# Kernel optimization log

Measured on AMD Instinct MI355X. Metric: run time of the kernel, lower is better.

## Reference

```python
import jax, jax.numpy as jnp
import numpy as np

OUT = 7       # roi_pooling_output_size
SR = 2        # bilinear samples per bin side (torchvision default is adaptive; fixed here)
STRIDES = (4, 8, 16, 32)
LEVELS = (2, 3, 4, 5)  # log2(strides)


def _roi_align(feat, boxes, bidx, scale):
    """roi_align, aligned=False. feat [B,C,H,W], boxes [N,4] xyxy image coords."""
    N = boxes.shape[0]
    C, H, W = feat.shape[1], feat.shape[2], feat.shape[3]
    x1 = boxes[:, 0] * scale; y1 = boxes[:, 1] * scale
    x2 = boxes[:, 2] * scale; y2 = boxes[:, 3] * scale
    rw = jnp.maximum(x2 - x1, 1.0); rh = jnp.maximum(y2 - y1, 1.0)
    g = (jnp.arange(SR, dtype=feat.dtype) + 0.5) / SR
    off = (jnp.arange(OUT, dtype=feat.dtype)[:, None] + g[None, :]).reshape(-1)  # [OUT*SR]
    ys = y1[:, None] + off[None, :] * (rh / OUT)[:, None]  # [N, OUT*SR]
    xs = x1[:, None] + off[None, :] * (rw / OUT)[:, None]
    M = OUT * SR
    y = jnp.broadcast_to(ys[:, :, None], (N, M, M)).reshape(N, M * M)
    x = jnp.broadcast_to(xs[:, None, :], (N, M, M)).reshape(N, M * M)
    valid = (y > -1.0) & (y < H) & (x > -1.0) & (x < W)
    y = jnp.clip(y, 0.0, H - 1); x = jnp.clip(x, 0.0, W - 1)
    y0f = jnp.floor(y); x0f = jnp.floor(x)
    y0 = y0f.astype(jnp.int32); x0 = x0f.astype(jnp.int32)
    yb = jnp.minimum(y0 + 1, H - 1); xb = jnp.minimum(x0 + 1, W - 1)
    ly = y - y0f; lx = x - x0f

    def gat(yi, xi):
        return feat[bidx[:, None], :, yi, xi]  # [N, P, C]

    v = (((1 - ly) * (1 - lx))[..., None] * gat(y0, x0)
         + ((1 - ly) * lx)[..., None] * gat(y0, xb)
         + (ly * (1 - lx))[..., None] * gat(yb, x0)
         + (ly * lx)[..., None] * gat(yb, xb))
    v = jnp.where(valid[..., None], v, 0.0)
    v = v.reshape(N, OUT, SR, OUT, SR, C).mean(axis=(2, 4))  # avg samples per bin
    return v.transpose(0, 3, 1, 2)  # [N, C, OUT, OUT]


def _forward(feat2, feat3, feat4, feat5, rois, W_fc1, b_fc1, W_fc2, b_fc2,
             W_cls, b_cls, W_reg, b_reg):
    feats = (feat2, feat3, feat4, feat5)
    BS, R = rois.shape[0], rois.shape[1]
    N = BS * R
    boxes = rois.reshape(N, 4)
    bidx = jnp.repeat(jnp.arange(BS, dtype=jnp.int32), R)
    w = boxes[:, 2] - boxes[:, 0]
    h = boxes[:, 3] - boxes[:, 1]
    # FPN level routing: floor(4 + log2(sqrt(wh)/224 + 1e-6)); unclamped, as in source
    lv = jnp.floor(4.0 + jnp.log2(jnp.sqrt(w * h) / 224.0 + 1e-6))
    C = feat2.shape[1]
    roi_feats = jnp.zeros((N, C, OUT, OUT), dtype=feat2.dtype)
    for f, s, l in zip(feats, STRIDES, LEVELS):
        rf = _roi_align(f, boxes, bidx, 1.0 / s)
        roi_feats = roi_feats + jnp.where((lv == l)[:, None, None, None], rf, 0.0)
    x = roi_feats.reshape(N, -1)                    # [N, 12544]
    x = jax.nn.relu(x @ W_fc1.T + b_fc1)            # roi_head fc1
    x = jax.nn.relu(x @ W_fc2.T + b_fc2)            # roi_head fc2
    cls_pred = (x @ W_cls.T + b_cls).reshape(BS, R, -1)
    reg_pred = (x @ W_reg.T + b_reg).reshape(BS, R, -1, 4)
    return cls_pred, reg_pred


def setup_inputs() -> dict:
    key = jax.random.key(0)
    ks = jax.random.split(key, 12)
    BS, R, C = 2, 512, 256
    IMG = 800.0
    inp = {}
    for i, (name, s) in enumerate(zip(['feat2', 'feat3', 'feat4', 'feat5'],
                                      [200, 100, 50, 25])):
        inp[name] = jax.random.normal(ks[i], (BS, C, s, s), dtype=jnp.float32)
    # realistic ROIs: uniform centers, log-uniform sizes in [32, 512] px
    ctr = jax.random.uniform(ks[4], (BS, R, 2), minval=0.0, maxval=IMG)
    sz = jnp.exp(jax.random.uniform(ks[5], (BS, R, 2),
                                    minval=jnp.log(32.0), maxval=jnp.log(512.0)))
    x1y1 = jnp.clip(ctr - sz / 2, 0.0, IMG)
    x2y2 = jnp.clip(ctr + sz / 2, 0.0, IMG)
    inp['rois'] = jnp.concatenate([x1y1, x2y2], axis=-1)
    D, F, NCLS = 1024, C * OUT * OUT, 80
    inp['W_fc1'] = 0.01 * jax.random.normal(ks[6], (D, F), dtype=jnp.float32)
    inp['b_fc1'] = jnp.zeros((D,), dtype=jnp.float32)
    inp['W_fc2'] = 0.01 * jax.random.normal(ks[7], (D, D), dtype=jnp.float32)
    inp['b_fc2'] = jnp.zeros((D,), dtype=jnp.float32)
    inp['W_cls'] = 0.01 * jax.random.normal(ks[8], (NCLS + 1, D), dtype=jnp.float32)
    inp['b_cls'] = jnp.zeros((NCLS + 1,), dtype=jnp.float32)
    inp['W_reg'] = 0.01 * jax.random.normal(ks[9], (NCLS * 4, D), dtype=jnp.float32)
    inp['b_reg'] = jnp.zeros((NCLS * 4,), dtype=jnp.float32)
    return inp


def reference(feat2, feat3, feat4, feat5, rois, W_fc1, b_fc1, W_fc2, b_fc2,
              W_cls, b_cls, W_reg, b_reg):
    return _forward(feat2, feat3, feat4, feat5, rois, W_fc1, b_fc1, W_fc2, b_fc2,
                    W_cls, b_cls, W_reg, b_reg)
```

## Files before the change

kernel.cpp:

```cpp
#include <hip/hip_runtime.h>

typedef __bf16 bf16_t;
typedef __bf16 bf16x8 __attribute__((ext_vector_type(8)));
typedef __bf16 bf16x4v __attribute__((ext_vector_type(4)));
typedef float f32x4 __attribute__((ext_vector_type(4)));

#define GLDS16(g, l)                                                            \
  __builtin_amdgcn_global_load_lds((const __attribute__((address_space(1))) void*)(g), \
                                   (__attribute__((address_space(3))) void*)(l), 16, 0, 0)

__global__ __launch_bounds__(256) void cvt_bf16_kernel(const float* __restrict__ x,
                                                       bf16_t* __restrict__ y, int n4) {
  int i = blockIdx.x * 256 + threadIdx.x;
  if (i >= n4) return;
  float4 v = ((const float4*)x)[i];
  union { bf16_t b[4]; uint2 u; } p;
  p.b[0] = (bf16_t)v.x; p.b[1] = (bf16_t)v.y; p.b[2] = (bf16_t)v.z; p.b[3] = (bf16_t)v.w;
  ((uint2*)y)[i] = p.u;
}

__global__ __launch_bounds__(256) void build_cat_kernel(const float* __restrict__ Wc,
                                                        const float* __restrict__ bc,
                                                        const float* __restrict__ Wr,
                                                        const float* __restrict__ br,
                                                        bf16_t* __restrict__ Wcat,
                                                        float* __restrict__ bcat) {
  int i = blockIdx.x * 256 + threadIdx.x;
  int row = i >> 10, col = i & 1023;
  float v = 0.0f;
  if (row < 81) v = Wc[row * 1024 + col];
  else if (row < 401) v = Wr[(row - 81) * 1024 + col];
  Wcat[i] = (bf16_t)v;
  if (i < 448) bcat[i] = (i < 81) ? bc[i] : ((i < 401) ? br[i - 81] : 0.0f);
}

__global__ __launch_bounds__(256) void nchw_to_nhwc_bf16(const float* __restrict__ src,
                                                         bf16_t* __restrict__ dst, int P) {
  __shared__ float tile[64 * 65];
  const int t = threadIdx.x;
  const int p0 = blockIdx.x * 64, c0 = blockIdx.y * 64, b = blockIdx.z;
  const float* s = src + (size_t)(b * 256 + c0) * P;
#pragma unroll
  for (int it = 0; it < 16; ++it) {
    const int ch = it * 4 + (t >> 6);
    const int px = t & 63;
    float v = 0.0f;
    if (p0 + px < P) v = s[(size_t)ch * P + p0 + px];
    tile[ch * 65 + px] = v;
  }
  __syncthreads();
  bf16_t* d = dst + ((size_t)b * P + p0) * 256 + c0;
#pragma unroll
  for (int it = 0; it < 4; ++it) {
    const int px = it * 16 + (t >> 4);
    const int ch4 = (t & 15) * 4;
    if (p0 + px < P) {
      union { bf16_t bb[4]; uint2 u; } pk;
#pragma unroll
      for (int k2 = 0; k2 < 4; k2++) pk.bb[k2] = (bf16_t)tile[(ch4 + k2) * 65 + px];
      *(uint2*)&d[(size_t)px * 256 + ch4] = pk.u;
    }
  }
}

__global__ __launch_bounds__(256) void permute_w1(const float* __restrict__ W1,
                                                  bf16_t* __restrict__ W1p) {
  __shared__ bf16_t lds[49 * 258];
  const int t = threadIdx.x;
  const float* src = W1 + (size_t)blockIdx.x * 12544;
  for (int it = 0; it < 49; ++it) {
    const int j = it * 256 + t;
    const int c = j / 49;
    const int bin = j - c * 49;
    lds[bin * 258 + c] = (bf16_t)src[j];
  }
  __syncthreads();
  bf16_t* dst = W1p + (size_t)blockIdx.x * 12544;
  for (int j4 = t; j4 < 3136; j4 += 256) {
    const int bin = j4 >> 6;
    const int c = (j4 & 63) * 4;
    union { bf16_t bb[4]; uint2 u; } pk;
#pragma unroll
    for (int k2 = 0; k2 < 4; k2++) pk.bb[k2] = lds[bin * 258 + c + k2];
    ((uint2*)dst)[j4] = pk.u;
  }
}

__global__ __launch_bounds__(256) void roi_align_nhwc(const bf16_t* __restrict__ fb2,
                                                      const bf16_t* __restrict__ fb3,
                                                      const bf16_t* __restrict__ fb4,
                                                      const bf16_t* __restrict__ fb5,
                                                      const float* __restrict__ rois,
                                                      bf16_t* __restrict__ A) {
  const int n = blockIdx.x;
  const int t = threadIdx.x;
  const int b = n >> 9;
  const float4 box = ((const float4*)rois)[n];
  const float w = box.z - box.x, h = box.w - box.y;
  const int lv = (int)floorf(4.0f + log2f(sqrtf(w * h) / 224.0f + 1e-6f));
  bf16_t* Ar = A + (size_t)n * 12544;

  if (lv < 2 || lv > 5) {
    uint2 z; z.x = 0; z.y = 0;
    for (int j = t; j < 3136; j += 256) ((uint2*)Ar)[j] = z;
    return;
  }

  const bf16_t* F; int H, W; float scale;
  if (lv == 2)      { F = fb2; H = 200; W = 200; scale = 0.25f; }
  else if (lv == 3) { F = fb3; H = 100; W = 100; scale = 0.125f; }
  else if (lv == 4) { F = fb4; H = 50;  W = 50;  scale = 0.0625f; }
  else              { F = fb5; H = 25;  W = 25;  scale = 0.03125f; }
  F += (size_t)b * H * W * 256;

  __shared__ int   s_x0[14], s_xb[14], s_y0w[14], s_ybw[14];
  __shared__ float s_wx0[14], s_wx1[14], s_wy0[14], s_wy1[14];

  const float x1s = box.x * scale, y1s = box.y * scale;
  const float x2s = box.z * scale, y2s = box.w * scale;
  const float rw = fmaxf(x2s - x1s, 1.0f), rh = fmaxf(y2s - y1s, 1.0f);
  const float bwx = rw * (1.0f / 7.0f), bwy = rh * (1.0f / 7.0f);

  if (t < 14) {
    const int i2 = t >> 1, j = t & 1;
    const float off = (float)i2 + ((float)j + 0.5f) * 0.5f;
    float x = x1s + off * bwx;
    float vx = (x > -1.0f && x < (float)W) ? 1.0f : 0.0f;
    x = fminf(fmaxf(x, 0.0f), (float)(W - 1));
    float x0f = floorf(x);
    int x0 = (int)x0f;
    s_x0[t] = x0; s_xb[t] = min(x0 + 1, W - 1);
    float lx = x - x0f;
    s_wx0[t] = (1.0f - lx) * vx; s_wx1[t] = lx * vx;
    float y = y1s + off * bwy;
    float vy = (y > -1.0f && y < (float)H) ? 1.0f : 0.0f;
    y = fminf(fmaxf(y, 0.0f), (float)(H - 1));
    float y0f = floorf(y);
    int y0 = (int)y0f;
    s_y0w[t] = y0 * W; s_ybw[t] = min(y0 + 1, H - 1) * W;
    float ly = y - y0f;
    s_wy0[t] = (1.0f - ly) * vy; s_wy1[t] = ly * vy;
  }
  __syncthreads();

  const int wv = t >> 6, l = t & 63;
  const int c4 = l * 4;
  for (int bin = wv; bin < 49; bin += 4) {
    const int by = bin / 7, bx = bin - by * 7;
    float a0 = 0, a1 = 0, a2 = 0, a3 = 0;
#pragma unroll
    for (int sa = 0; sa < 2; sa++) {
      const int my = 2 * by + sa;
      const int y0w = s_y0w[my], ybw = s_ybw[my];
      const float wy0 = s_wy0[my], wy1 = s_wy1[my];
#pragma unroll
      for (int sb = 0; sb < 2; sb++) {
        const int mx = 2 * bx + sb;
        const int x0 = s_x0[mx], xb = s_xb[mx];
        const float w00 = wy0 * s_wx0[mx], w01 = wy0 * s_wx1[mx];
        const float w10 = wy1 * s_wx0[mx], w11 = wy1 * s_wx1[mx];
        bf16x4v v00 = *(const bf16x4v*)&F[(size_t)(y0w + x0) * 256 + c4];
        bf16x4v v01 = *(const bf16x4v*)&F[(size_t)(y0w + xb) * 256 + c4];
        bf16x4v v10 = *(const bf16x4v*)&F[(size_t)(ybw + x0) * 256 + c4];
        bf16x4v v11 = *(const bf16x4v*)&F[(size_t)(ybw + xb) * 256 + c4];
        a0 += w00 * (float)v00[0] + w01 * (float)v01[0] + w10 * (float)v10[0] + w11 * (float)v11[0];
        a1 += w00 * (float)v00[1] + w01 * (float)v01[1] + w10 * (float)v10[1] + w11 * (float)v11[1];
        a2 += w00 * (float)v00[2] + w01 * (float)v01[2] + w10 * (float)v10[2] + w11 * (float)v11[2];
        a3 += w00 * (float)v00[3] + w01 * (float)v01[3] + w10 * (float)v10[3] + w11 * (float)v11[3];
      }
    }
    union { bf16_t bb[4]; uint2 u; } pk;
    pk.bb[0] = (bf16_t)(a0 * 0.25f);
    pk.bb[1] = (bf16_t)(a1 * 0.25f);
    pk.bb[2] = (bf16_t)(a2 * 0.25f);
    pk.bb[3] = (bf16_t)(a3 * 0.25f);
    *(uint2*)&Ar[bin * 256 + c4] = pk.u;
  }
}

__global__ __launch_bounds__(256, 2) void gemm1_splitk(const bf16_t* __restrict__ A,
                                                       const bf16_t* __restrict__ B,
                                                       float* __restrict__ Cp) {
  __shared__ __align__(16) bf16_t As[128 * 32];
  __shared__ __align__(16) bf16_t Bs[128 * 32];
  const int t = threadIdx.x;
  const int w = t >> 6, l = t & 63;
  const int bm = blockIdx.x * 128, bn = blockIdx.y * 128;
  const int K = 12544;
  const int k0 = blockIdx.z * 1568;
  const int row1 = t >> 2, kc = (t & 3) * 8;
  const bf16_t* gA1 = A + (size_t)(bm + row1) * K + k0 + kc;
  const bf16_t* gA2 = gA1 + (size_t)64 * K;
  const bf16_t* gB1 = B + (size_t)(bn + row1) * K + k0 + kc;
  const bf16_t* gB2 = gB1 + (size_t)64 * K;
  bf16_t* lA1 = As + w * 512;
  bf16_t* lA2 = As + 2048 + w * 512;
  bf16_t* lB1 = Bs + w * 512;
  bf16_t* lB2 = Bs + 2048 + w * 512;
  const int wm = (w >> 1) * 64, wn = (w & 1) * 64;
  const int rA = l & 15, kq = (l >> 4) * 8;
  f32x4 acc[4][4] = {};

  for (int kk = 0; kk < 49; ++kk) {
    GLDS16(gA1, lA1); GLDS16(gA2, lA2);
    GLDS16(gB1, lB1); GLDS16(gB2, lB2);
    gA1 += 32; gA2 += 32; gB1 += 32; gB2 += 32;
    __syncthreads();
    bf16x8 a[4], b[4];
#pragma unroll
    for (int i = 0; i < 4; i++) {
      a[i] = *(const bf16x8*)&As[(wm + i * 16 + rA) * 32 + kq];
      b[i] = *(const bf16x8*)&Bs[(wn + i * 16 + rA) * 32 + kq];
    }
#pragma unroll
    for (int i = 0; i < 4; i++)
#pragma unroll
      for (int j = 0; j < 4; j++)
        acc[i][j] = __builtin_amdgcn_mfma_f32_16x16x32_bf16(a[i], b[j], acc[i][j], 0, 0, 0);
    __syncthreads();
  }

  const int q = l >> 4, cc = l & 15;
  float* Co = Cp + ((size_t)blockIdx.z << 20);
#pragma unroll
  for (int i = 0; i < 4; i++) {
#pragma unroll
    for (int j = 0; j < 4; j++) {
      const int col = bn + wn + j * 16 + cc;
      const int r0 = bm + wm + i * 16 + q * 4;
#pragma unroll
      for (int r = 0; r < 4; r++)
        Co[(size_t)(r0 + r) * 1024 + col] = acc[i][j][r];
    }
  }
}

__global__ __launch_bounds__(256) void reduce_fc1(const float* __restrict__ Cp,
                                                  const float* __restrict__ bias,
                                                  bf16_t* __restrict__ X) {
  const int i4 = blockIdx.x * 256 + threadIdx.x;
  const float4* C4 = (const float4*)Cp;
  float4 s = C4[i4];
#pragma unroll
  for (int z = 1; z < 8; z++) {
    float4 v = C4[(size_t)z * 262144 + i4];
    s.x += v.x; s.y += v.y; s.z += v.z; s.w += v.w;
  }
  const float4 bv = *(const float4*)&bias[(i4 & 255) * 4];
  union { bf16_t bb[4]; uint2 u; } pk;
  pk.bb[0] = (bf16_t)fmaxf(s.x + bv.x, 0.0f);
  pk.bb[1] = (bf16_t)fmaxf(s.y + bv.y, 0.0f);
  pk.bb[2] = (bf16_t)fmaxf(s.z + bv.z, 0.0f);
  pk.bb[3] = (bf16_t)fmaxf(s.w + bv.w, 0.0f);
  ((uint2*)X)[i4] = pk.u;
}

template <int MODE>
__global__ __launch_bounds__(256) void gemm_bt(const bf16_t* __restrict__ A,
                                               const bf16_t* __restrict__ B,
                                               const float* __restrict__ bias,
                                               void* __restrict__ out,
                                               int M, int N, int K) {
  __shared__ __align__(16) bf16_t As[64 * 32];
  __shared__ __align__(16) bf16_t Bs[64 * 32];
  const int t = threadIdx.x;
  const int wv = t >> 6, l = t & 63;
  const int bm = blockIdx.x * 64, bn = blockIdx.y * 64;
  const int wm = (wv >> 1) * 32, wn = (wv & 1) * 32;

  const int srow = t >> 2;
  const int skc = (t & 3) * 8;
  const bf16_t* ga = A + (size_t)(bm + srow) * K + skc;
  const bf16_t* gb = B + (size_t)(bn + srow) * K + skc;

  uint4 ra = *(const uint4*)ga;
  uint4 rb = *(const uint4*)gb;
  f32x4 acc[2][2] = {};

  const int nIter = K >> 5;
  const int rA = l & 15;
  const int kq = (l >> 4) << 3;
  for (int i = 0; i < nIter; ++i) {
    ga += 32; gb += 32;
    *(uint4*)&As[srow * 32 + skc] = ra;
    *(uint4*)&Bs[srow * 32 + skc] = rb;
    __syncthreads();
    if (i + 1 < nIter) { ra = *(const uint4*)ga; rb = *(const uint4*)gb; }
    bf16x8 a0 = *(const bf16x8*)&As[(wm + rA) * 32 + kq];
    bf16x8 a1 = *(const bf16x8*)&As[(wm + 16 + rA) * 32 + kq];
    bf16x8 b0 = *(const bf16x8*)&Bs[(wn + rA) * 32 + kq];
    bf16x8 b1 = *(const bf16x8*)&Bs[(wn + 16 + rA) * 32 + kq];
    acc[0][0] = __builtin_amdgcn_mfma_f32_16x16x32_bf16(a0, b0, acc[0][0], 0, 0, 0);
    acc[0][1] = __builtin_amdgcn_mfma_f32_16x16x32_bf16(a0, b1, acc[0][1], 0, 0, 0);
    acc[1][0] = __builtin_amdgcn_mfma_f32_16x16x32_bf16(a1, b0, acc[1][0], 0, 0, 0);
    acc[1][1] = __builtin_amdgcn_mfma_f32_16x16x32_bf16(a1, b1, acc[1][1], 0, 0, 0);
    __syncthreads();
  }

  const int q = l >> 4;
  const int cc = l & 15;
#pragma unroll
  for (int i2 = 0; i2 < 2; i2++) {
#pragma unroll
    for (int j2 = 0; j2 < 2; j2++) {
      const int col = bn + wn + j2 * 16 + cc;
      const int row0 = bm + wm + i2 * 16 + q * 4;
      const float bv = bias[col];
#pragma unroll
      for (int r = 0; r < 4; r++) {
        float v = acc[i2][j2][r] + bv;
        const int row = row0 + r;
        if (MODE == 0) {
          v = fmaxf(v, 0.0f);
          ((bf16_t*)out)[(size_t)row * N + col] = (bf16_t)v;
        } else {
          if (col < 81)       ((float*)out)[(size_t)row * 81 + col] = v;
          else if (col < 401) ((float*)out)[82944 + (size_t)row * 320 + (col - 81)] = v;
        }
      }
    }
  }
}

extern "C" void kernel_launch(void* const* d_in, const int* in_sizes, int n_in,
                              void* d_out, int out_size, void* d_ws, size_t ws_size,
                              hipStream_t stream) {
  const float* f2   = (const float*)d_in[0];
  const float* f3   = (const float*)d_in[1];
  const float* f4   = (const float*)d_in[2];
  const float* f5   = (const float*)d_in[3];
  const float* rois = (const float*)d_in[4];
  const float* W1   = (const float*)d_in[5];
  const float* b1   = (const float*)d_in[6];
  const float* W2   = (const float*)d_in[7];
  const float* b2   = (const float*)d_in[8];
  const float* Wc   = (const float*)d_in[9];
  const float* bc   = (const float*)d_in[10];
  const float* Wr   = (const float*)d_in[11];
  const float* br   = (const float*)d_in[12];

  char* ws = (char*)d_ws;
  bf16_t* Ab   = (bf16_t*)(ws);
  bf16_t* W1b  = (bf16_t*)(ws + 25690112);
  bf16_t* X1b  = (bf16_t*)(ws + 51380224);
  bf16_t* W2b  = (bf16_t*)(ws + 53477376);
  bf16_t* X2b  = (bf16_t*)(ws + 55574528);
  bf16_t* Wcb  = (bf16_t*)(ws + 57671680);
  float*  bcat = (float*)(ws + 58589184);
  bf16_t* FT   = (bf16_t*)(ws + 58591232);
  float*  Cp   = (float*)(ws + 58591232);
  bf16_t* FT2 = FT;
  bf16_t* FT3 = FT + 20480000;
  bf16_t* FT4 = FT + 25600000;
  bf16_t* FT5 = FT + 26880000;

  nchw_to_nhwc_bf16<<<dim3(625, 4, 2), 256, 0, stream>>>(f2, FT2, 40000);
  nchw_to_nhwc_bf16<<<dim3(157, 4, 2), 256, 0, stream>>>(f3, FT3, 10000);
  nchw_to_nhwc_bf16<<<dim3(40, 4, 2), 256, 0, stream>>>(f4, FT4, 2500);
  nchw_to_nhwc_bf16<<<dim3(10, 4, 2), 256, 0, stream>>>(f5, FT5, 625);
  cvt_bf16_kernel<<<1024, 256, 0, stream>>>(W2, W2b, 262144);
  build_cat_kernel<<<1792, 256, 0, stream>>>(Wc, bc, Wr, br, Wcb, bcat);
  permute_w1<<<1024, 256, 0, stream>>>(W1, W1b);
  roi_align_nhwc<<<1024, 256, 0, stream>>>(FT2, FT3, FT4, FT5, rois, Ab);

  gemm1_splitk<<<dim3(8, 8, 8), 256, 0, stream>>>(Ab, W1b, Cp);
  reduce_fc1<<<1024, 256, 0, stream>>>(Cp, b1, X1b);
  gemm_bt<0><<<dim3(16, 16), 256, 0, stream>>>(X1b, W2b, b2, (void*)X2b, 1024, 1024, 1024);
  gemm_bt<1><<<dim3(16, 7), 256, 0, stream>>>(X2b, Wcb, bcat, d_out, 1024, 448, 1024);
}
```

Baseline: 355.0 us.

## Merge prep kernels, fuse split-K reduction into GEMM1, swizzle LDS layouts

All preprocessing launches (feature transposes, W1 permute, W2 and classifier weight conversion, counter reset) are merged into one kernel that dispatches on block index. The separate split-K reduce kernel is removed. The last block to finish each output tile, found with an atomic counter, now sums the partials and applies bias and ReLU. An XOR swizzle of the LDS k-chunk offsets is added in both GEMMs to cut bank conflicts. These changes target launch overhead, an extra pass over the partial buffer and LDS conflicts, at the cost of threadfence/atomic ordering and a serialized tail for the last block per tile.

```diff
diff --git a/kernel.cpp b/kernel.cpp
--- a/kernel.cpp
+++ b/kernel.cpp
@@ -9,80 +9,98 @@
   __builtin_amdgcn_global_load_lds((const __attribute__((address_space(1))) void*)(g), \
                                    (__attribute__((address_space(3))) void*)(l), 16, 0, 0)
 
-__global__ __launch_bounds__(256) void cvt_bf16_kernel(const float* __restrict__ x,
-                                                       bf16_t* __restrict__ y, int n4) {
-  int i = blockIdx.x * 256 + threadIdx.x;
-  if (i >= n4) return;
-  float4 v = ((const float4*)x)[i];
-  union { bf16_t b[4]; uint2 u; } p;
-  p.b[0] = (bf16_t)v.x; p.b[1] = (bf16_t)v.y; p.b[2] = (bf16_t)v.z; p.b[3] = (bf16_t)v.w;
-  ((uint2*)y)[i] = p.u;
-}
-
-__global__ __launch_bounds__(256) void build_cat_kernel(const float* __restrict__ Wc,
-                                                        const float* __restrict__ bc,
-                                                        const float* __restrict__ Wr,
-                                                        const float* __restrict__ br,
-                                                        bf16_t* __restrict__ Wcat,
-                                                        float* __restrict__ bcat) {
-  int i = blockIdx.x * 256 + threadIdx.x;
-  int row = i >> 10, col = i & 1023;
-  float v = 0.0f;
-  if (row < 81) v = Wc[row * 1024 + col];
-  else if (row < 401) v = Wr[(row - 81) * 1024 + col];
-  Wcat[i] = (bf16_t)v;
-  if (i < 448) bcat[i] = (i < 81) ? bc[i] : ((i < 401) ? br[i - 81] : 0.0f);
-}
-
-__global__ __launch_bounds__(256) void nchw_to_nhwc_bf16(const float* __restrict__ src,
-                                                         bf16_t* __restrict__ dst, int P) {
-  __shared__ float tile[64 * 65];
+__global__ __launch_bounds__(256) void prep_all(const float* __restrict__ f2,
+                                                const float* __restrict__ f3,
+                                                const float* __restrict__ f4,
+                                                const float* __restrict__ f5,
+                                                const float* __restrict__ W1,
+                                                const float* __restrict__ W2,
+                                                const float* __restrict__ Wc,
+                                                const float* __restrict__ bc,
+                                                const float* __restrict__ Wr,
+                                                const float* __restrict__ br,
+                                                bf16_t* __restrict__ FT2,
+                                                bf16_t* __restrict__ FT3,
+                                                bf16_t* __restrict__ FT4,
+                                                bf16_t* __restrict__ FT5,
+                                                bf16_t* __restrict__ W1p,
+                                                bf16_t* __restrict__ W2b,
+                                                bf16_t* __restrict__ Wcb,
+                                                float* __restrict__ bcat,
+                                                int* __restrict__ cnt) {
+  __shared__ __align__(16) char smraw[25344];
+  const int bid = blockIdx.x;
   const int t = threadIdx.x;
-  const int p0 = blockIdx.x * 64, c0 = blockIdx.y * 64, b = blockIdx.z;
-  const float* s = src + (size_t)(b * 256 + c0) * P;
-#pragma unroll
-  for (int it = 0; it < 16; ++it) {
-    const int ch = it * 4 + (t >> 6);
-    const int px = t & 63;
+
+  if (bid < 6656) {
+    float* tile = (float*)smraw;
+    const float* src; bf16_t* dst; int P, rel, ptiles;
+    if (bid < 5000)      { src = f2; dst = FT2; P = 40000; rel = bid;        ptiles = 625; }
+    else if (bid < 6256) { src = f3; dst = FT3; P = 10000; rel = bid - 5000; ptiles = 157; }
+    else if (bid < 6576) { src = f4; dst = FT4; P = 2500;  rel = bid - 6256; ptiles = 40; }
+    else                 { src = f5; dst = FT5; P = 625;   rel = bid - 6576; ptiles = 10; }
+    const int pt = rel % ptiles;
+    const int cb = (rel / ptiles) & 3;
+    const int b = rel / (ptiles * 4);
+    const int p0 = pt * 64, c0 = cb * 64;
+    const float* s = src + (size_t)(b * 256 + c0) * P;
+#pragma unroll
+    for (int it = 0; it < 16; ++it) {
+      const int ch = it * 4 + (t >> 6);
+      const int px = t & 63;
+      float v = 0.0f;
+      if (p0 + px < P) v = s[(size_t)ch * P + p0 + px];
+      tile[ch * 65 + px] = v;
+    }
+    __syncthreads();
+    bf16_t* d = dst + ((size_t)b * P + p0) * 256 + c0;
+#pragma unroll
+    for (int it = 0; it < 4; ++it) {
+      const int px = it * 16 + (t >> 4);
+      const int ch4 = (t & 15) * 4;
+      if (p0 + px < P) {
+        union { bf16_t bb[4]; uint2 u; } pk;
+#pragma unroll
+        for (int k2 = 0; k2 < 4; k2++) pk.bb[k2] = (bf16_t)tile[(ch4 + k2) * 65 + px];
+        *(uint2*)&d[(size_t)px * 256 + ch4] = pk.u;
+      }
+    }
+  } else if (bid < 7680) {
+    bf16_t* pw = (bf16_t*)smraw;
+    const int row = bid - 6656;
+    const float* src = W1 + (size_t)row * 12544;
+    for (int it = 0; it < 49; ++it) {
+      const int j = it * 256 + t;
+      const int c = j / 49;
+      const int bin = j - c * 49;
+      pw[bin * 258 + c] = (bf16_t)src[j];
+    }
+    __syncthreads();
+    bf16_t* dst = W1p + (size_t)row * 12544;
+    for (int j4 = t; j4 < 3136; j4 += 256) {
+      const int bin = j4 >> 6;
+      const int c = (j4 & 63) * 4;
+      union { bf16_t bb[4]; uint2 u; } pk;
+#pragma unroll
+      for (int k2 = 0; k2 < 4; k2++) pk.bb[k2] = pw[bin * 258 + c + k2];
+      ((uint2*)dst)[j4] = pk.u;
+    }
+  } else if (bid < 8704) {
+    const int i = (bid - 7680) * 256 + t;
+    float4 v = ((const float4*)W2)[i];
+    union { bf16_t b[4]; uint2 u; } p;
+    p.b[0] = (bf16_t)v.x; p.b[1] = (bf16_t)v.y; p.b[2] = (bf16_t)v.z; p.b[3] = (bf16_t)v.w;
+    ((uint2*)W2b)[i] = p.u;
+  } else if (bid < 10496) {
+    const int i = (bid - 8704) * 256 + t;
+    const int row = i >> 10, col = i & 1023;
     float v = 0.0f;
-    if (p0 + px < P) v = s[(size_t)ch * P + p0 + px];
-    tile[ch * 65 + px] = v;
-  }
-  __syncthreads();
-  bf16_t* d = dst + ((size_t)b * P + p0) * 256 + c0;
-#pragma unroll
-  for (int it = 0; it < 4; ++it) {
-    const int px = it * 16 + (t >> 4);
-    const int ch4 = (t & 15) * 4;
-    if (p0 + px < P) {
-      union { bf16_t bb[4]; uint2 u; } pk;
-#pragma unroll
-      for (int k2 = 0; k2 < 4; k2++) pk.bb[k2] = (bf16_t)tile[(ch4 + k2) * 65 + px];
-      *(uint2*)&d[(size_t)px * 256 + ch4] = pk.u;
-    }
-  }
-}
-
-__global__ __launch_bounds__(256) void permute_w1(const float* __restrict__ W1,
-                                                  bf16_t* __restrict__ W1p) {
-  __shared__ bf16_t lds[49 * 258];
-  const int t = threadIdx.x;
-  const float* src = W1 + (size_t)blockIdx.x * 12544;
-  for (int it = 0; it < 49; ++it) {
-    const int j = it * 256 + t;
-    const int c = j / 49;
-    const int bin = j - c * 49;
-    lds[bin * 258 + c] = (bf16_t)src[j];
-  }
-  __syncthreads();
-  bf16_t* dst = W1p + (size_t)blockIdx.x * 12544;
-  for (int j4 = t; j4 < 3136; j4 += 256) {
-    const int bin = j4 >> 6;
-    const int c = (j4 & 63) * 4;
-    union { bf16_t bb[4]; uint2 u; } pk;
-#pragma unroll
-    for (int k2 = 0; k2 < 4; k2++) pk.bb[k2] = lds[bin * 258 + c + k2];
-    ((uint2*)dst)[j4] = pk.u;
+    if (row < 81) v = Wc[row * 1024 + col];
+    else if (row < 401) v = Wr[(row - 81) * 1024 + col];
+    Wcb[i] = (bf16_t)v;
+    if (i < 448) bcat[i] = (i < 81) ? bc[i] : ((i < 401) ? br[i - 81] : 0.0f);
+  } else {
+    if (t < 64) cnt[t] = 0;
   }
 }
 
@@ -180,15 +198,20 @@
 
 __global__ __launch_bounds__(256, 2) void gemm1_splitk(const bf16_t* __restrict__ A,
                                                        const bf16_t* __restrict__ B,
-                                                       float* __restrict__ Cp) {
+                                                       const float* __restrict__ bias,
+                                                       float* __restrict__ Cp,
+                                                       bf16_t* __restrict__ X,
+                                                       int* __restrict__ cnt) {
   __shared__ __align__(16) bf16_t As[128 * 32];
   __shared__ __align__(16) bf16_t Bs[128 * 32];
   const int t = threadIdx.x;
   const int w = t >> 6, l = t & 63;
   const int bm = blockIdx.x * 128, bn = blockIdx.y * 128;
+  const int bz = blockIdx.z;
   const int K = 12544;
-  const int k0 = blockIdx.z * 1568;
-  const int row1 = t >> 2, kc = (t & 3) * 8;
+  const int k0 = bz * 1568;
+  const int row1 = t >> 2;
+  const int kc = ((t & 3) ^ ((t >> 3) & 3)) * 8;
   const bf16_t* gA1 = A + (size_t)(bm + row1) * K + k0 + kc;
   const bf16_t* gA2 = gA1 + (size_t)64 * K;
   const bf16_t* gB1 = B + (size_t)(bn + row1) * K + k0 + kc;
@@ -198,7 +221,8 @@
   bf16_t* lB1 = Bs + w * 512;
   bf16_t* lB2 = Bs + 2048 + w * 512;
   const int wm = (w >> 1) * 64, wn = (w & 1) * 64;
-  const int rA = l & 15, kq = (l >> 4) * 8;
+  const int rA = l & 15;
+  const int kqs = (((l >> 4) ^ ((rA >> 1) & 3))) * 8;
   f32x4 acc[4][4] = {};
 
   for (int kk = 0; kk < 49; ++kk) {
@@ -209,8 +233,8 @@
     bf16x8 a[4], b[4];
 #pragma unroll
     for (int i = 0; i < 4; i++) {
-      a[i] = *(const bf16x8*)&As[(wm + i * 16 + rA) * 32 + kq];
-      b[i] = *(const bf16x8*)&Bs[(wn + i * 16 + rA) * 32 + kq];
+      a[i] = *(const bf16x8*)&As[(wm + i * 16 + rA) * 32 + kqs];
+      b[i] = *(const bf16x8*)&Bs[(wn + i * 16 + rA) * 32 + kqs];
     }
 #pragma unroll
     for (int i = 0; i < 4; i++)
@@ -221,9 +245,9 @@
   }
 
   const int q = l >> 4, cc = l & 15;
-  float* Co = Cp + ((size_t)blockIdx.z << 20);
-#pragma unroll
-  for (int i = 0; i < 4; i++) {
+  float* Co = Cp + ((size_t)bz << 20);
+#pragma unroll
+  for (int i = 0; i < 4; i++)
 #pragma unroll
     for (int j = 0; j < 4; j++) {
       const int col = bn + wn + j * 16 + cc;
@@ -232,27 +256,34 @@
       for (int r = 0; r < 4; r++)
         Co[(size_t)(r0 + r) * 1024 + col] = acc[i][j][r];
     }
-  }
-}
-
-__global__ __launch_bounds__(256) void reduce_fc1(const float* __restrict__ Cp,
-                                                  const float* __restrict__ bias,
-                                                  bf16_t* __restrict__ X) {
-  const int i4 = blockIdx.x * 256 + threadIdx.x;
-  const float4* C4 = (const float4*)Cp;
-  float4 s = C4[i4];
-#pragma unroll
-  for (int z = 1; z < 8; z++) {
-    float4 v = C4[(size_t)z * 262144 + i4];
-    s.x += v.x; s.y += v.y; s.z += v.z; s.w += v.w;
-  }
-  const float4 bv = *(const float4*)&bias[(i4 & 255) * 4];
-  union { bf16_t bb[4]; uint2 u; } pk;
-  pk.bb[0] = (bf16_t)fmaxf(s.x + bv.x, 0.0f);
-  pk.bb[1] = (bf16_t)fmaxf(s.y + bv.y, 0.0f);
-  pk.bb[2] = (bf16_t)fmaxf(s.z + bv.z, 0.0f);
-  pk.bb[3] = (bf16_t)fmaxf(s.w + bv.w, 0.0f);
-  ((uint2*)X)[i4] = pk.u;
+
+  __threadfence();
+  __shared__ int s_last;
+  if (t == 0) {
+    int old = atomicAdd(&cnt[blockIdx.y * 8 + blockIdx.x], 1);
+    s_last = (old == 7) ? 1 : 0;
+  }
+  __syncthreads();
+  if (!s_last) return;
+  __threadfence();
+
+#pragma unroll
+  for (int i = 0; i < 4; i++)
+#pragma unroll
+    for (int j = 0; j < 4; j++) {
+      const int col = bn + wn + j * 16 + cc;
+      const int r0 = bm + wm + i * 16 + q * 4;
+      const float bv = bias[col];
+#pragma unroll
+      for (int r = 0; r < 4; r++) {
+        float v = acc[i][j][r];
+        const size_t off = (size_t)(r0 + r) * 1024 + col;
+        for (int z2 = 0; z2 < 8; z2++)
+          if (z2 != bz) v += Cp[((size_t)z2 << 20) + off];
+        v = fmaxf(v + bv, 0.0f);
+        X[off] = (bf16_t)v;
+      }
+    }
 }
 
 template <int MODE>
@@ -270,6 +301,7 @@
 
   const int srow = t >> 2;
   const int skc = (t & 3) * 8;
+  const int sst = ((t & 3) ^ ((t >> 3) & 3)) * 8;
   const bf16_t* ga = A + (size_t)(bm + srow) * K + skc;
   const bf16_t* gb = B + (size_t)(bn + srow) * K + skc;
 
@@ -279,17 +311,17 @@
 
   const int nIter = K >> 5;
   const int rA = l & 15;
-  const int kq = (l >> 4) << 3;
+  const int kqs = (((l >> 4) ^ ((rA >> 1) & 3))) * 8;
   for (int i = 0; i < nIter; ++i) {
     ga += 32; gb += 32;
-    *(uint4*)&As[srow * 32 + skc] = ra;
-    *(uint4*)&Bs[srow * 32 + skc] = rb;
+    *(uint4*)&As[srow * 32 + sst] = ra;
+    *(uint4*)&Bs[srow * 32 + sst] = rb;
     __syncthreads();
     if (i + 1 < nIter) { ra = *(const uint4*)ga; rb = *(const uint4*)gb; }
-    bf16x8 a0 = *(const bf16x8*)&As[(wm + rA) * 32 + kq];
-    bf16x8 a1 = *(const bf16x8*)&As[(wm + 16 + rA) * 32 + kq];
-    bf16x8 b0 = *(const bf16x8*)&Bs[(wn + rA) * 32 + kq];
-    bf16x8 b1 = *(const bf16x8*)&Bs[(wn + 16 + rA) * 32 + kq];
+    bf16x8 a0 = *(const bf16x8*)&As[(wm + rA) * 32 + kqs];
+    bf16x8 a1 = *(const bf16x8*)&As[(wm + 16 + rA) * 32 + kqs];
+    bf16x8 b0 = *(const bf16x8*)&Bs[(wn + rA) * 32 + kqs];
+    bf16x8 b1 = *(const bf16x8*)&Bs[(wn + 16 + rA) * 32 + kqs];
     acc[0][0] = __builtin_amdgcn_mfma_f32_16x16x32_bf16(a0, b0, acc[0][0], 0, 0, 0);
     acc[0][1] = __builtin_amdgcn_mfma_f32_16x16x32_bf16(a0, b1, acc[0][1], 0, 0, 0);
     acc[1][0] = __builtin_amdgcn_mfma_f32_16x16x32_bf16(a1, b0, acc[1][0], 0, 0, 0);
@@ -347,6 +379,7 @@
   bf16_t* X2b  = (bf16_t*)(ws + 55574528);
   bf16_t* Wcb  = (bf16_t*)(ws + 57671680);
   float*  bcat = (float*)(ws + 58589184);
+  int*    cnt  = (int*)(ws + 58590976);
   bf16_t* FT   = (bf16_t*)(ws + 58591232);
   float*  Cp   = (float*)(ws + 58591232);
   bf16_t* FT2 = FT;
@@ -354,17 +387,10 @@
   bf16_t* FT4 = FT + 25600000;
   bf16_t* FT5 = FT + 26880000;
 
-  nchw_to_nhwc_bf16<<<dim3(625, 4, 2), 256, 0, stream>>>(f2, FT2, 40000);
-  nchw_to_nhwc_bf16<<<dim3(157, 4, 2), 256, 0, stream>>>(f3, FT3, 10000);
-  nchw_to_nhwc_bf16<<<dim3(40, 4, 2), 256, 0, stream>>>(f4, FT4, 2500);
-  nchw_to_nhwc_bf16<<<dim3(10, 4, 2), 256, 0, stream>>>(f5, FT5, 625);
-  cvt_bf16_kernel<<<1024, 256, 0, stream>>>(W2, W2b, 262144);
-  build_cat_kernel<<<1792, 256, 0, stream>>>(Wc, bc, Wr, br, Wcb, bcat);
-  permute_w1<<<1024, 256, 0, stream>>>(W1, W1b);
+  prep_all<<<10497, 256, 0, stream>>>(f2, f3, f4, f5, W1, W2, Wc, bc, Wr, br,
+                                      FT2, FT3, FT4, FT5, W1b, W2b, Wcb, bcat, cnt);
   roi_align_nhwc<<<1024, 256, 0, stream>>>(FT2, FT3, FT4, FT5, rois, Ab);
-
-  gemm1_splitk<<<dim3(8, 8, 8), 256, 0, stream>>>(Ab, W1b, Cp);
-  reduce_fc1<<<1024, 256, 0, stream>>>(Cp, b1, X1b);
+  gemm1_splitk<<<dim3(8, 8, 8), 256, 0, stream>>>(Ab, W1b, b1, Cp, X1b, cnt);
   gemm_bt<0><<<dim3(16, 16), 256, 0, stream>>>(X1b, W2b, b2, (void*)X2b, 1024, 1024, 1024);
   gemm_bt<1><<<dim3(16, 7), 256, 0, stream>>>(X2b, Wcb, bcat, d_out, 1024, 448, 1024);
 }
```

New measurement: 489.4 us. +37.9%, slower.
